# Optimization experiments

Measured on AMD Instinct MI355X. Metric: run time of the kernel, lower is better.

## Reference

```python
import jax, jax.numpy as jnp
import numpy as np

B, S, D = 4, 2048, 1024
CTX_LEN, CTX_DIM = 77, 768
H, DH = 16, 64
INNER = H * DH
MULT = 4
EPS = 1e-5


def setup_inputs() -> dict:
    key = jax.random.key(0)
    ks = jax.random.split(key, 14)
    nrm = lambda k, shape: jax.random.normal(k, shape, dtype=jnp.float32) * 0.02
    return {
        "x": jax.random.normal(ks[0], (B, S, D), dtype=jnp.float32),
        "context": jax.random.normal(ks[1], (B, CTX_LEN, CTX_DIM), dtype=jnp.float32),
        "ln1_g": jnp.ones((D,), jnp.float32), "ln1_b": jnp.zeros((D,), jnp.float32),
        "ln2_g": jnp.ones((D,), jnp.float32), "ln2_b": jnp.zeros((D,), jnp.float32),
        "ln3_g": jnp.ones((D,), jnp.float32), "ln3_b": jnp.zeros((D,), jnp.float32),
        "a1_wq": nrm(ks[2], (D, INNER)), "a1_wk": nrm(ks[3], (D, INNER)),
        "a1_wv": nrm(ks[4], (D, INNER)), "a1_wo": nrm(ks[5], (INNER, D)),
        "a1_bo": jnp.zeros((D,), jnp.float32),
        "a2_wq": nrm(ks[6], (D, INNER)), "a2_wk": nrm(ks[7], (CTX_DIM, INNER)),
        "a2_wv": nrm(ks[8], (CTX_DIM, INNER)), "a2_wo": nrm(ks[9], (INNER, D)),
        "a2_bo": jnp.zeros((D,), jnp.float32),
        "ff_w1": nrm(ks[10], (D, D * MULT * 2)), "ff_b1": jnp.zeros((D * MULT * 2,), jnp.float32),
        "ff_w2": nrm(ks[11], (D * MULT, D)), "ff_b2": jnp.zeros((D,), jnp.float32),
    }


def _layernorm(x, g, b):
    mu = jnp.mean(x, axis=-1, keepdims=True)
    var = jnp.var(x, axis=-1, keepdims=True)
    return (x - mu) * jax.lax.rsqrt(var + EPS) * g + b


def _attn(xq, xkv, wq, wk, wv, wo, bo):
    b, sq, _ = xq.shape
    sk = xkv.shape[1]
    q = (xq @ wq).reshape(b, sq, H, DH)
    k = (xkv @ wk).reshape(b, sk, H, DH)
    v = (xkv @ wv).reshape(b, sk, H, DH)
    score = jnp.einsum('bqhd,bkhd->bhqk', q, k) * (DH ** -0.5)
    w = jax.nn.softmax(score, axis=-1)
    o = jnp.einsum('bhqk,bkhd->bqhd', w, v).reshape(b, sq, INNER)
    return o @ wo + bo


def _block(x, context, ln1_g, ln1_b, ln2_g, ln2_b, ln3_g, ln3_b,
           a1_wq, a1_wk, a1_wv, a1_wo, a1_bo,
           a2_wq, a2_wk, a2_wv, a2_wo, a2_bo,
           ff_w1, ff_b1, ff_w2, ff_b2):
    # self-attention
    x = _attn(_layernorm(x, ln1_g, ln1_b), _layernorm(x, ln1_g, ln1_b),
              a1_wq, a1_wk, a1_wv, a1_wo, a1_bo) + x
    # cross-attention
    x = _attn(_layernorm(x, ln2_g, ln2_b), context,
              a2_wq, a2_wk, a2_wv, a2_wo, a2_bo) + x
    # GeGLU feed-forward
    h = _layernorm(x, ln3_g, ln3_b) @ ff_w1 + ff_b1
    u, gate = jnp.split(h, 2, axis=-1)
    x = (u * jax.nn.gelu(gate, approximate=False)) @ ff_w2 + ff_b2 + x
    return x


def reference(x, context, ln1_g, ln1_b, ln2_g, ln2_b, ln3_g, ln3_b,
              a1_wq, a1_wk, a1_wv, a1_wo, a1_bo,
              a2_wq, a2_wk, a2_wv, a2_wo, a2_bo,
              ff_w1, ff_b1, ff_w2, ff_b2):
    return _block(x, context, ln1_g, ln1_b, ln2_g, ln2_b, ln3_g, ln3_b,
                  a1_wq, a1_wk, a1_wv, a1_wo, a1_bo,
                  a2_wq, a2_wk, a2_wv, a2_wo, a2_bo,
                  ff_w1, ff_b1, ff_w2, ff_b2)
```

## Files before the change

### kernel.cpp

```cpp
#include <hip/hip_runtime.h>
#include <hip/hip_bf16.h>
#include <math.h>

typedef __bf16 bf16;
typedef __bf16 bf16x8 __attribute__((ext_vector_type(8)));
typedef float f32x4 __attribute__((ext_vector_type(4)));

#define MFMA(a, b, c) __builtin_amdgcn_mfma_f32_16x16x32_bf16((a), (b), (c), 0, 0, 0)

static __device__ __forceinline__ void gl16(const bf16* g, bf16* l) {
  __builtin_amdgcn_global_load_lds(
      (const __attribute__((address_space(1))) void*)g,
      (__attribute__((address_space(3))) void*)l, 16, 0, 0);
}

static __device__ __forceinline__ bf16x8 bzero8() {
  bf16x8 v;
#pragma unroll
  for (int i = 0; i < 8; ++i) v[i] = (bf16)0.0f;
  return v;
}

__global__ void k_transpose_cvt(const float* __restrict__ W, bf16* __restrict__ Wt,
                                int K, int N) {
  __shared__ float tile[32][33];
  int k0 = blockIdx.x * 32, n0 = blockIdx.y * 32;
  int tx = threadIdx.x & 31, ty = threadIdx.x >> 5;
  for (int i = ty; i < 32; i += 8)
    tile[i][tx] = W[(size_t)(k0 + i) * N + (n0 + tx)];
  __syncthreads();
  for (int i = ty; i < 32; i += 8)
    Wt[(size_t)(n0 + i) * K + (k0 + tx)] = (bf16)tile[tx][i];
}

__global__ void k_cvt(const float* __restrict__ in, bf16* __restrict__ out, int n) {
  int i = blockIdx.x * 256 + threadIdx.x;
  if (i < n) out[i] = (bf16)in[i];
}

__global__ void k_layernorm(const float* __restrict__ x, const float* __restrict__ g,
                            const float* __restrict__ b, bf16* __restrict__ out) {
  int row = blockIdx.x;
  float4 v = ((const float4*)(x + (size_t)row * 1024))[threadIdx.x];
  float s = v.x + v.y + v.z + v.w;
  float ss = v.x * v.x + v.y * v.y + v.z * v.z + v.w * v.w;
#pragma unroll
  for (int off = 1; off < 64; off <<= 1) {
    s += __shfl_xor(s, off);
    ss += __shfl_xor(ss, off);
  }
  __shared__ float sm[4], sm2[4];
  int w = threadIdx.x >> 6;
  if ((threadIdx.x & 63) == 0) { sm[w] = s; sm2[w] = ss; }
  __syncthreads();
  s = sm[0] + sm[1] + sm[2] + sm[3];
  ss = sm2[0] + sm2[1] + sm2[2] + sm2[3];
  float mu = s * (1.0f / 1024.0f);
  float var = ss * (1.0f / 1024.0f) - mu * mu;
  float rs = rsqrtf(var + 1e-5f);
  float4 gg = ((const float4*)g)[threadIdx.x];
  float4 bb = ((const float4*)b)[threadIdx.x];
  bf16* o = out + (size_t)row * 1024 + threadIdx.x * 4;
  o[0] = (bf16)((v.x - mu) * rs * gg.x + bb.x);
  o[1] = (bf16)((v.y - mu) * rs * gg.y + bb.y);
  o[2] = (bf16)((v.z - mu) * rs * gg.z + bb.z);
  o[3] = (bf16)((v.w - mu) * rs * gg.w + bb.w);
}

template <int EPI>
__global__ __launch_bounds__(256, 2)
void k_gemm_bt(const bf16* __restrict__ A, const bf16* __restrict__ Bt,
               const float* __restrict__ bias, const float* __restrict__ res,
               void* __restrict__ Cp, int M, int N, int K) {
  __shared__ __attribute__((aligned(16))) bf16 As[128 * 32];
  __shared__ __attribute__((aligned(16))) bf16 Bs[128 * 32];
  int m0 = blockIdx.x * 128, n0 = blockIdx.y * 128;
  int tid = threadIdx.x, lane = tid & 63, wave = tid >> 6;
  int wm = (wave >> 1) * 64, wn = (wave & 1) * 64;
  int quad = lane >> 4, l15 = lane & 15;
  f32x4 acc[4][4];
#pragma unroll
  for (int i = 0; i < 4; ++i)
#pragma unroll
    for (int j = 0; j < 4; ++j)
#pragma unroll
      for (int r = 0; r < 4; ++r) acc[i][j][r] = 0.0f;
  int srow = wave * 16 + (lane >> 2), scol = (lane & 3) * 8;
  const bf16* ga = A + (size_t)(m0 + srow) * K + scol;
  const bf16* gb = Bt + (size_t)(n0 + srow) * K + scol;
  bf16* la = As + srow * 32 + scol;
  bf16* lb = Bs + srow * 32 + scol;
  for (int k0 = 0; k0 < K; k0 += 32) {
    gl16(ga, la);
    gl16(ga + (size_t)64 * K, la + 64 * 32);
    gl16(gb, lb);
    gl16(gb + (size_t)64 * K, lb + 64 * 32);
    ga += 32; gb += 32;
    __syncthreads();
    bf16x8 af[4], bfr[4];
#pragma unroll
    for (int i = 0; i < 4; ++i) af[i] = *(const bf16x8*)(&As[(wm + i * 16 + l15) * 32 + quad * 8]);
#pragma unroll
    for (int i = 0; i < 4; ++i) bfr[i] = *(const bf16x8*)(&Bs[(wn + i * 16 + l15) * 32 + quad * 8]);
#pragma unroll
    for (int mi = 0; mi < 4; ++mi)
#pragma unroll
      for (int ni = 0; ni < 4; ++ni)
        acc[mi][ni] = MFMA(af[mi], bfr[ni], acc[mi][ni]);
    __syncthreads();
  }
#pragma unroll
  for (int mi = 0; mi < 4; ++mi) {
#pragma unroll
    for (int r = 0; r < 4; ++r) {
      int row = m0 + wm + mi * 16 + quad * 4 + r;
      if (row >= M) continue;
#pragma unroll
      for (int ni = 0; ni < 4; ++ni) {
        int col = n0 + wn + ni * 16 + l15;
        float v = acc[mi][ni][r];
        if (EPI == 0) {
          ((bf16*)Cp)[(size_t)row * N + col] = (bf16)v;
        } else {
          ((float*)Cp)[(size_t)row * N + col] =
              v + bias[col] + res[(size_t)row * N + col];
        }
      }
    }
  }
}

__global__ __launch_bounds__(256, 2)
void k_gemm_geglu(const bf16* __restrict__ A, const bf16* __restrict__ W1t,
                  const float* __restrict__ b1, bf16* __restrict__ Hg,
                  int M, int K) {
  __shared__ __attribute__((aligned(16))) bf16 As[128 * 32];
  __shared__ __attribute__((aligned(16))) bf16 Bu[64 * 32];
  __shared__ __attribute__((aligned(16))) bf16 Bg[64 * 32];
  const int N = 4096;
  int m0 = blockIdx.x * 128, n0 = blockIdx.y * 64;
  int tid = threadIdx.x, lane = tid & 63, wave = tid >> 6;
  int wm = (wave >> 1) * 64, wn = (wave & 1) * 32;
  int quad = lane >> 4, l15 = lane & 15;
  f32x4 accu[4][2], accg[4][2];
#pragma unroll
  for (int i = 0; i < 4; ++i)
#pragma unroll
    for (int j = 0; j < 2; ++j)
#pragma unroll
      for (int r = 0; r < 4; ++r) { accu[i][j][r] = 0.0f; accg[i][j][r] = 0.0f; }
  int srow = wave * 16 + (lane >> 2), scol = (lane & 3) * 8;
  const bf16* ga = A + (size_t)(m0 + srow) * K + scol;
  const bf16* gu = W1t + (size_t)(n0 + srow) * K + scol;
  const bf16* gg = W1t + (size_t)(n0 + srow + 4096) * K + scol;
  bf16* la = As + srow * 32 + scol;
  bf16* lu = Bu + srow * 32 + scol;
  bf16* lg = Bg + srow * 32 + scol;
  for (int k0 = 0; k0 < K; k0 += 32) {
    gl16(ga, la);
    gl16(ga + (size_t)64 * K, la + 64 * 32);
    gl16(gu, lu);
    gl16(gg, lg);
    ga += 32; gu += 32; gg += 32;
    __syncthreads();
    bf16x8 af[4], bu[2], bg[2];
#pragma unroll
    for (int i = 0; i < 4; ++i) af[i] = *(const bf16x8*)(&As[(wm + i * 16 + l15) * 32 + quad * 8]);
#pragma unroll
    for (int i = 0; i < 2; ++i) bu[i] = *(const bf16x8*)(&Bu[(wn + i * 16 + l15) * 32 + quad * 8]);
#pragma unroll
    for (int i = 0; i < 2; ++i) bg[i] = *(const bf16x8*)(&Bg[(wn + i * 16 + l15) * 32 + quad * 8]);
#pragma unroll
    for (int mi = 0; mi < 4; ++mi)
#pragma unroll
      for (int ni = 0; ni < 2; ++ni) {
        accu[mi][ni] = MFMA(af[mi], bu[ni], accu[mi][ni]);
        accg[mi][ni] = MFMA(af[mi], bg[ni], accg[mi][ni]);
      }
    __syncthreads();
  }
#pragma unroll
  for (int mi = 0; mi < 4; ++mi)
#pragma unroll
    for (int r = 0; r < 4; ++r) {
      int row = m0 + wm + mi * 16 + quad * 4 + r;
#pragma unroll
      for (int ni = 0; ni < 2; ++ni) {
        int col = n0 + wn + ni * 16 + l15;
        float u = accu[mi][ni][r] + b1[col];
        float g = accg[mi][ni][r] + b1[col + 4096];
        float ge = 0.5f * g * (1.0f + erff(g * 0.70710678118654752f));
        Hg[(size_t)row * N + col] = (bf16)(u * ge);
      }
    }
}

__global__ __launch_bounds__(256, 2)
void k_flash(const bf16* __restrict__ Q, const bf16* __restrict__ Kb,
             const bf16* __restrict__ Vb, bf16* __restrict__ O,
             int Sq, int Sk, int kvrows) {
  __shared__ __attribute__((aligned(16))) bf16 Qs[64][72];
  __shared__ __attribute__((aligned(16))) bf16 Ks[64][72];
  __shared__ __attribute__((aligned(16))) bf16 Vt[64][72];
  __shared__ __attribute__((aligned(16))) bf16 Ps[4][16][72];
  int qt = blockIdx.x, h = blockIdx.y, b = blockIdx.z;
  int tid = threadIdx.x, lane = tid & 63, wave = tid >> 6;
  int quad = lane >> 4, l15 = lane & 15;
  {
    int r = tid >> 2, c0 = (tid & 3) * 16;
    const bf16* src = Q + (size_t)(b * Sq + qt * 64 + r) * 1024 + h * 64 + c0;
    *(bf16x8*)(&Qs[r][c0]) = *(const bf16x8*)(src);
    *(bf16x8*)(&Qs[r][c0 + 8]) = *(const bf16x8*)(src + 8);
  }
  float m_r[4], l_r[4];
  f32x4 acc_o[4];
#pragma unroll
  for (int r = 0; r < 4; ++r) { m_r[r] = -1e30f; l_r[r] = 0.0f; }
#pragma unroll
  for (int ni = 0; ni < 4; ++ni)
#pragma unroll
    for (int r = 0; r < 4; ++r) acc_o[ni][r] = 0.0f;

  for (int k0 = 0; k0 < Sk; k0 += 64) {
    {
      int r = tid >> 2, c0 = (tid & 3) * 16;
      int krow = k0 + r;
      bf16x8 k1 = bzero8(), k2 = bzero8(), v1 = bzero8(), v2 = bzero8();
      if (krow < Sk) {
        const bf16* ks = Kb + (size_t)(b * kvrows + krow) * 1024 + h * 64 + c0;
        k1 = *(const bf16x8*)ks;
        k2 = *(const bf16x8*)(ks + 8);
        const bf16* vs = Vb + (size_t)(b * kvrows + krow) * 1024 + h * 64 + c0;
        v1 = *(const bf16x8*)vs;
        v2 = *(const bf16x8*)(vs + 8);
      }
      *(bf16x8*)(&Ks[r][c0]) = k1;
      *(bf16x8*)(&Ks[r][c0 + 8]) = k2;
#pragma unroll
      for (int j = 0; j < 8; ++j) { Vt[c0 + j][r] = v1[j]; Vt[c0 + 8 + j][r] = v2[j]; }
    }
    __syncthreads();

    f32x4 sacc[4];
#pragma unroll
    for (int ni = 0; ni < 4; ++ni)
#pragma unroll
      for (int r = 0; r < 4; ++r) sacc[ni][r] = 0.0f;
#pragma unroll
    for (int ks = 0; ks < 2; ++ks) {
      bf16x8 aq = *(const bf16x8*)(&Qs[wave * 16 + l15][ks * 32 + quad * 8]);
#pragma unroll
      for (int ni = 0; ni < 4; ++ni) {
        bf16x8 bk = *(const bf16x8*)(&Ks[ni * 16 + l15][ks * 32 + quad * 8]);
        sacc[ni] = MFMA(aq, bk, sacc[ni]);
      }
    }
    float s_v[4][4];
#pragma unroll
    for (int ni = 0; ni < 4; ++ni)
#pragma unroll
      for (int r = 0; r < 4; ++r) {
        float sv = sacc[ni][r] * 0.125f;
        if (k0 + ni * 16 + l15 >= Sk) sv = -1e30f;
        s_v[ni][r] = sv;
      }
    float alpha[4];
#pragma unroll
    for (int r = 0; r < 4; ++r) {
      float v = fmaxf(fmaxf(s_v[0][r], s_v[1][r]), fmaxf(s_v[2][r], s_v[3][r]));
#pragma unroll
      for (int off = 1; off < 16; off <<= 1) v = fmaxf(v, __shfl_xor(v, off));
      float mn = fmaxf(m_r[r], v);
      alpha[r] = __expf(m_r[r] - mn);
      m_r[r] = mn;
    }
    float p_v[4][4];
#pragma unroll
    for (int ni = 0; ni < 4; ++ni)
#pragma unroll
      for (int r = 0; r < 4; ++r) p_v[ni][r] = __expf(s_v[ni][r] - m_r[r]);
#pragma unroll
    for (int r = 0; r < 4; ++r) {
      float v = p_v[0][r] + p_v[1][r] + p_v[2][r] + p_v[3][r];
#pragma unroll
      for (int off = 1; off < 16; off <<= 1) v += __shfl_xor(v, off);
      l_r[r] = l_r[r] * alpha[r] + v;
    }
#pragma unroll
    for (int ni = 0; ni < 4; ++ni)
#pragma unroll
      for (int r = 0; r < 4; ++r) acc_o[ni][r] *= alpha[r];
#pragma unroll
    for (int ni = 0; ni < 4; ++ni)
#pragma unroll
      for (int r = 0; r < 4; ++r)
        Ps[wave][quad * 4 + r][ni * 16 + l15] = (bf16)p_v[ni][r];
#pragma unroll
    for (int ks = 0; ks < 2; ++ks) {
      bf16x8 ap = *(const bf16x8*)(&Ps[wave][l15][ks * 32 + quad * 8]);
#pragma unroll
      for (int ni = 0; ni < 4; ++ni) {
        bf16x8 bv = *(const bf16x8*)(&Vt[ni * 16 + l15][ks * 32 + quad * 8]);
        acc_o[ni] = MFMA(ap, bv, acc_o[ni]);
      }
    }
    __syncthreads();
  }
#pragma unroll
  for (int ni = 0; ni < 4; ++ni)
#pragma unroll
    for (int r = 0; r < 4; ++r) {
      int q = qt * 64 + wave * 16 + quad * 4 + r;
      float ov = acc_o[ni][r] / l_r[r];
      O[(size_t)(b * Sq + q) * 1024 + h * 64 + ni * 16 + l15] = (bf16)ov;
    }
}

extern "C" void kernel_launch(void* const* d_in, const int* in_sizes, int n_in,
                              void* d_out, int out_size, void* d_ws, size_t ws_size,
                              hipStream_t stream) {
  (void)in_sizes; (void)n_in; (void)out_size; (void)ws_size;
  const float* x = (const float*)d_in[0];
  const float* ctx = (const float*)d_in[1];
  const float* ln1_g = (const float*)d_in[2];
  const float* ln1_b = (const float*)d_in[3];
  const float* ln2_g = (const float*)d_in[4];
  const float* ln2_b = (const float*)d_in[5];
  const float* ln3_g = (const float*)d_in[6];
  const float* ln3_b = (const float*)d_in[7];
  const float* a1_wq = (const float*)d_in[8];
  const float* a1_wk = (const float*)d_in[9];
  const float* a1_wv = (const float*)d_in[10];
  const float* a1_wo = (const float*)d_in[11];
  const float* a1_bo = (const float*)d_in[12];
  const float* a2_wq = (const float*)d_in[13];
  const float* a2_wk = (const float*)d_in[14];
  const float* a2_wv = (const float*)d_in[15];
  const float* a2_wo = (const float*)d_in[16];
  const float* a2_bo = (const float*)d_in[17];
  const float* ff_w1 = (const float*)d_in[18];
  const float* ff_b1 = (const float*)d_in[19];
  const float* ff_w2 = (const float*)d_in[20];
  const float* ff_b2 = (const float*)d_in[21];
  float* xout = (float*)d_out;

  const int M = 4 * 2048;
  char* ws = (char*)d_ws;
  size_t off = 0;
  auto alloc = [&](size_t elems) -> bf16* {
    bf16* p = (bf16*)(ws + off);
    off += ((elems * sizeof(bf16)) + 255) & ~(size_t)255;
    return p;
  };
  bf16* wq1t = alloc((size_t)1024 * 1024);
  bf16* wk1t = alloc((size_t)1024 * 1024);
  bf16* wv1t = alloc((size_t)1024 * 1024);
  bf16* wo1t = alloc((size_t)1024 * 1024);
  bf16* wq2t = alloc((size_t)1024 * 1024);
  bf16* wk2t = alloc((size_t)1024 * 768);
  bf16* wv2t = alloc((size_t)1024 * 768);
  bf16* wo2t = alloc((size_t)1024 * 1024);
  bf16* w1t = alloc((size_t)8192 * 1024);
  bf16* w2t = alloc((size_t)1024 * 4096);
  bf16* lnb = alloc((size_t)M * 1024);
  bf16* qb = alloc((size_t)M * 1024);
  bf16* kb = alloc((size_t)M * 1024);
  bf16* vb = alloc((size_t)M * 1024);
  bf16* ab = alloc((size_t)M * 1024);
  bf16* ctxb = alloc((size_t)308 * 768);
  bf16* kcb = alloc((size_t)308 * 1024);
  bf16* vcb = alloc((size_t)308 * 1024);
  bf16* hgb = alloc((size_t)M * 4096);

  hipMemcpyAsync(xout, x, (size_t)M * 1024 * sizeof(float),
                 hipMemcpyDeviceToDevice, stream);

  k_transpose_cvt<<<dim3(32, 32), 256, 0, stream>>>(a1_wq, wq1t, 1024, 1024);
  k_transpose_cvt<<<dim3(32, 32), 256, 0, stream>>>(a1_wk, wk1t, 1024, 1024);
  k_transpose_cvt<<<dim3(32, 32), 256, 0, stream>>>(a1_wv, wv1t, 1024, 1024);
  k_transpose_cvt<<<dim3(32, 32), 256, 0, stream>>>(a1_wo, wo1t, 1024, 1024);
  k_transpose_cvt<<<dim3(32, 32), 256, 0, stream>>>(a2_wq, wq2t, 1024, 1024);
  k_transpose_cvt<<<dim3(24, 32), 256, 0, stream>>>(a2_wk, wk2t, 768, 1024);
  k_transpose_cvt<<<dim3(24, 32), 256, 0, stream>>>(a2_wv, wv2t, 768, 1024);
  k_transpose_cvt<<<dim3(32, 32), 256, 0, stream>>>(a2_wo, wo2t, 1024, 1024);
  k_transpose_cvt<<<dim3(32, 256), 256, 0, stream>>>(ff_w1, w1t, 1024, 8192);
  k_transpose_cvt<<<dim3(128, 32), 256, 0, stream>>>(ff_w2, w2t, 4096, 1024);
  k_cvt<<<(308 * 768 + 255) / 256, 256, 0, stream>>>(ctx, ctxb, 308 * 768);

  k_layernorm<<<M, 256, 0, stream>>>(xout, ln1_g, ln1_b, lnb);
  k_gemm_bt<0><<<dim3(64, 8), 256, 0, stream>>>(lnb, wq1t, nullptr, nullptr, qb, M, 1024, 1024);
  k_gemm_bt<0><<<dim3(64, 8), 256, 0, stream>>>(lnb, wk1t, nullptr, nullptr, kb, M, 1024, 1024);
  k_gemm_bt<0><<<dim3(64, 8), 256, 0, stream>>>(lnb, wv1t, nullptr, nullptr, vb, M, 1024, 1024);
  k_flash<<<dim3(32, 16, 4), 256, 0, stream>>>(qb, kb, vb, ab, 2048, 2048, 2048);
  k_gemm_bt<1><<<dim3(64, 8), 256, 0, stream>>>(ab, wo1t, a1_bo, xout, xout, M, 1024, 1024);

  k_layernorm<<<M, 256, 0, stream>>>(xout, ln2_g, ln2_b, lnb);
  k_gemm_bt<0><<<dim3(64, 8), 256, 0, stream>>>(lnb, wq2t, nullptr, nullptr, qb, M, 1024, 1024);
  k_gemm_bt<0><<<dim3(3, 8), 256, 0, stream>>>(ctxb, wk2t, nullptr, nullptr, kcb, 308, 1024, 768);
  k_gemm_bt<0><<<dim3(3, 8), 256, 0, stream>>>(ctxb, wv2t, nullptr, nullptr, vcb, 308, 1024, 768);
  k_flash<<<dim3(32, 16, 4), 256, 0, stream>>>(qb, kcb, vcb, ab, 2048, 77, 77);
  k_gemm_bt<1><<<dim3(64, 8), 256, 0, stream>>>(ab, wo2t, a2_bo, xout, xout, M, 1024, 1024);

  k_layernorm<<<M, 256, 0, stream>>>(xout, ln3_g, ln3_b, lnb);
  k_gemm_geglu<<<dim3(64, 64), 256, 0, stream>>>(lnb, w1t, ff_b1, hgb, M, 1024);
  k_gemm_bt<1><<<dim3(64, 8), 256, 0, stream>>>(hgb, w2t, ff_b2, xout, xout, M, 1024, 4096);
}
```

Measured before the change: 990.1 us.

## Pre-transpose V globally, keep Q in registers, widen GeGLU tile, MFMA row sums

A new kernel transposes V into a per-head [d][token] layout held in the GeGLU scratch buffer. Flash attention can then load V tiles with vector copies instead of scalar transposed LDS stores. Flash also keeps Q fragments in registers, dropping the Q LDS tile, and computes softmax row sums with an MFMA against a ones vector instead of shuffles. The GeGLU GEMM tile grows to 128 columns, which doubles accumulators per wave and may lower occupancy, and the extra transpose launch adds traffic.

```diff
diff --git a/kernel.cpp b/kernel.cpp
--- a/kernel.cpp
+++ b/kernel.cpp
@@ -31,6 +31,31 @@
   __syncthreads();
   for (int i = ty; i < 32; i += 8)
     Wt[(size_t)(n0 + i) * K + (k0 + tx)] = (bf16)tile[tx][i];
+}
+
+__global__ void k_transpose_v(const bf16* __restrict__ V, bf16* __restrict__ Vt,
+                              int rows, int kvpad) {
+  __shared__ __attribute__((aligned(16))) bf16 tile[64][72];
+  int t0 = blockIdx.x * 64, h = blockIdx.y, b = blockIdx.z;
+  int t = threadIdx.x;
+  int tr = t >> 2, c0 = (t & 3) * 16;
+  int token = t0 + tr;
+  bf16x8 a = bzero8(), bv = bzero8();
+  if (token < rows) {
+    const bf16* src = V + ((size_t)(b * rows + token)) * 1024 + h * 64 + c0;
+    a = *(const bf16x8*)src;
+    bv = *(const bf16x8*)(src + 8);
+  }
+  *(bf16x8*)&tile[tr][c0] = a;
+  *(bf16x8*)&tile[tr][c0 + 8] = bv;
+  __syncthreads();
+  int d = t >> 2, tq = (t & 3) * 16;
+  bf16x8 o1, o2;
+#pragma unroll
+  for (int i = 0; i < 8; ++i) { o1[i] = tile[tq + i][d]; o2[i] = tile[tq + 8 + i][d]; }
+  bf16* dst = Vt + ((size_t)((b * 16 + h) * 64 + d)) * kvpad + t0 + tq;
+  *(bf16x8*)dst = o1;
+  *(bf16x8*)(dst + 8) = o2;
 }
 
 __global__ void k_cvt(const float* __restrict__ in, bf16* __restrict__ out, int n) {
@@ -135,18 +160,18 @@
                   const float* __restrict__ b1, bf16* __restrict__ Hg,
                   int M, int K) {
   __shared__ __attribute__((aligned(16))) bf16 As[128 * 32];
-  __shared__ __attribute__((aligned(16))) bf16 Bu[64 * 32];
-  __shared__ __attribute__((aligned(16))) bf16 Bg[64 * 32];
+  __shared__ __attribute__((aligned(16))) bf16 Bu[128 * 32];
+  __shared__ __attribute__((aligned(16))) bf16 Bg[128 * 32];
   const int N = 4096;
-  int m0 = blockIdx.x * 128, n0 = blockIdx.y * 64;
+  int m0 = blockIdx.x * 128, n0 = blockIdx.y * 128;
   int tid = threadIdx.x, lane = tid & 63, wave = tid >> 6;
-  int wm = (wave >> 1) * 64, wn = (wave & 1) * 32;
+  int wm = (wave >> 1) * 64, wn = (wave & 1) * 64;
   int quad = lane >> 4, l15 = lane & 15;
-  f32x4 accu[4][2], accg[4][2];
+  f32x4 accu[4][4], accg[4][4];
 #pragma unroll
   for (int i = 0; i < 4; ++i)
 #pragma unroll
-    for (int j = 0; j < 2; ++j)
+    for (int j = 0; j < 4; ++j)
 #pragma unroll
       for (int r = 0; r < 4; ++r) { accu[i][j][r] = 0.0f; accg[i][j][r] = 0.0f; }
   int srow = wave * 16 + (lane >> 2), scol = (lane & 3) * 8;
@@ -160,20 +185,22 @@
     gl16(ga, la);
     gl16(ga + (size_t)64 * K, la + 64 * 32);
     gl16(gu, lu);
+    gl16(gu + (size_t)64 * K, lu + 64 * 32);
     gl16(gg, lg);
+    gl16(gg + (size_t)64 * K, lg + 64 * 32);
     ga += 32; gu += 32; gg += 32;
     __syncthreads();
-    bf16x8 af[4], bu[2], bg[2];
+    bf16x8 af[4], bu[4], bg[4];
 #pragma unroll
     for (int i = 0; i < 4; ++i) af[i] = *(const bf16x8*)(&As[(wm + i * 16 + l15) * 32 + quad * 8]);
 #pragma unroll
-    for (int i = 0; i < 2; ++i) bu[i] = *(const bf16x8*)(&Bu[(wn + i * 16 + l15) * 32 + quad * 8]);
-#pragma unroll
-    for (int i = 0; i < 2; ++i) bg[i] = *(const bf16x8*)(&Bg[(wn + i * 16 + l15) * 32 + quad * 8]);
+    for (int i = 0; i < 4; ++i) bu[i] = *(const bf16x8*)(&Bu[(wn + i * 16 + l15) * 32 + quad * 8]);
+#pragma unroll
+    for (int i = 0; i < 4; ++i) bg[i] = *(const bf16x8*)(&Bg[(wn + i * 16 + l15) * 32 + quad * 8]);
 #pragma unroll
     for (int mi = 0; mi < 4; ++mi)
 #pragma unroll
-      for (int ni = 0; ni < 2; ++ni) {
+      for (int ni = 0; ni < 4; ++ni) {
         accu[mi][ni] = MFMA(af[mi], bu[ni], accu[mi][ni]);
         accg[mi][ni] = MFMA(af[mi], bg[ni], accg[mi][ni]);
       }
@@ -185,7 +212,7 @@
     for (int r = 0; r < 4; ++r) {
       int row = m0 + wm + mi * 16 + quad * 4 + r;
 #pragma unroll
-      for (int ni = 0; ni < 2; ++ni) {
+      for (int ni = 0; ni < 4; ++ni) {
         int col = n0 + wn + ni * 16 + l15;
         float u = accu[mi][ni][r] + b1[col];
         float g = accg[mi][ni][r] + b1[col + 4096];
@@ -197,21 +224,21 @@
 
 __global__ __launch_bounds__(256, 2)
 void k_flash(const bf16* __restrict__ Q, const bf16* __restrict__ Kb,
-             const bf16* __restrict__ Vb, bf16* __restrict__ O,
-             int Sq, int Sk, int kvrows) {
-  __shared__ __attribute__((aligned(16))) bf16 Qs[64][72];
+             const bf16* __restrict__ VtG, bf16* __restrict__ O,
+             int Sq, int Sk, int kvrows, int kvpad) {
   __shared__ __attribute__((aligned(16))) bf16 Ks[64][72];
-  __shared__ __attribute__((aligned(16))) bf16 Vt[64][72];
+  __shared__ __attribute__((aligned(16))) bf16 Vs[64][72];
   __shared__ __attribute__((aligned(16))) bf16 Ps[4][16][72];
   int qt = blockIdx.x, h = blockIdx.y, b = blockIdx.z;
   int tid = threadIdx.x, lane = tid & 63, wave = tid >> 6;
   int quad = lane >> 4, l15 = lane & 15;
-  {
-    int r = tid >> 2, c0 = (tid & 3) * 16;
-    const bf16* src = Q + (size_t)(b * Sq + qt * 64 + r) * 1024 + h * 64 + c0;
-    *(bf16x8*)(&Qs[r][c0]) = *(const bf16x8*)(src);
-    *(bf16x8*)(&Qs[r][c0 + 8]) = *(const bf16x8*)(src + 8);
-  }
+  const bf16* qsrc = Q + (size_t)(b * Sq + qt * 64 + wave * 16 + l15) * 1024 + h * 64 + quad * 8;
+  bf16x8 aq0 = *(const bf16x8*)qsrc;
+  bf16x8 aq1 = *(const bf16x8*)(qsrc + 32);
+  bf16x8 ones8;
+#pragma unroll
+  for (int i = 0; i < 8; ++i) ones8[i] = (bf16)1.0f;
+
   float m_r[4], l_r[4];
   f32x4 acc_o[4];
 #pragma unroll
@@ -221,23 +248,24 @@
 #pragma unroll
     for (int r = 0; r < 4; ++r) acc_o[ni][r] = 0.0f;
 
+  int tr = tid >> 2, c0 = (tid & 3) * 16;
+  const bf16* vrow = VtG + ((size_t)((b * 16 + h) * 64 + tr)) * kvpad + c0;
+
   for (int k0 = 0; k0 < Sk; k0 += 64) {
     {
-      int r = tid >> 2, c0 = (tid & 3) * 16;
-      int krow = k0 + r;
-      bf16x8 k1 = bzero8(), k2 = bzero8(), v1 = bzero8(), v2 = bzero8();
+      int krow = k0 + tr;
+      bf16x8 k1 = bzero8(), k2 = bzero8();
       if (krow < Sk) {
         const bf16* ks = Kb + (size_t)(b * kvrows + krow) * 1024 + h * 64 + c0;
         k1 = *(const bf16x8*)ks;
         k2 = *(const bf16x8*)(ks + 8);
-        const bf16* vs = Vb + (size_t)(b * kvrows + krow) * 1024 + h * 64 + c0;
-        v1 = *(const bf16x8*)vs;
-        v2 = *(const bf16x8*)(vs + 8);
       }
-      *(bf16x8*)(&Ks[r][c0]) = k1;
-      *(bf16x8*)(&Ks[r][c0 + 8]) = k2;
-#pragma unroll
-      for (int j = 0; j < 8; ++j) { Vt[c0 + j][r] = v1[j]; Vt[c0 + 8 + j][r] = v2[j]; }
+      *(bf16x8*)(&Ks[tr][c0]) = k1;
+      *(bf16x8*)(&Ks[tr][c0 + 8]) = k2;
+      bf16x8 v1 = *(const bf16x8*)(vrow + k0);
+      bf16x8 v2 = *(const bf16x8*)(vrow + k0 + 8);
+      *(bf16x8*)(&Vs[tr][c0]) = v1;
+      *(bf16x8*)(&Vs[tr][c0 + 8]) = v2;
     }
     __syncthreads();
 
@@ -247,13 +275,11 @@
 #pragma unroll
       for (int r = 0; r < 4; ++r) sacc[ni][r] = 0.0f;
 #pragma unroll
-    for (int ks = 0; ks < 2; ++ks) {
-      bf16x8 aq = *(const bf16x8*)(&Qs[wave * 16 + l15][ks * 32 + quad * 8]);
-#pragma unroll
-      for (int ni = 0; ni < 4; ++ni) {
-        bf16x8 bk = *(const bf16x8*)(&Ks[ni * 16 + l15][ks * 32 + quad * 8]);
-        sacc[ni] = MFMA(aq, bk, sacc[ni]);
-      }
+    for (int ni = 0; ni < 4; ++ni) {
+      bf16x8 bk0 = *(const bf16x8*)(&Ks[ni * 16 + l15][quad * 8]);
+      bf16x8 bk1 = *(const bf16x8*)(&Ks[ni * 16 + l15][32 + quad * 8]);
+      sacc[ni] = MFMA(aq0, bk0, sacc[ni]);
+      sacc[ni] = MFMA(aq1, bk1, sacc[ni]);
     }
     float s_v[4][4];
 #pragma unroll
@@ -274,35 +300,28 @@
       alpha[r] = __expf(m_r[r] - mn);
       m_r[r] = mn;
     }
-    float p_v[4][4];
 #pragma unroll
     for (int ni = 0; ni < 4; ++ni)
 #pragma unroll
-      for (int r = 0; r < 4; ++r) p_v[ni][r] = __expf(s_v[ni][r] - m_r[r]);
-#pragma unroll
-    for (int r = 0; r < 4; ++r) {
-      float v = p_v[0][r] + p_v[1][r] + p_v[2][r] + p_v[3][r];
-#pragma unroll
-      for (int off = 1; off < 16; off <<= 1) v += __shfl_xor(v, off);
-      l_r[r] = l_r[r] * alpha[r] + v;
-    }
-#pragma unroll
-    for (int ni = 0; ni < 4; ++ni)
+      for (int r = 0; r < 4; ++r)
+        Ps[wave][quad * 4 + r][ni * 16 + l15] = (bf16)__expf(s_v[ni][r] - m_r[r]);
+    bf16x8 ap0 = *(const bf16x8*)(&Ps[wave][l15][quad * 8]);
+    bf16x8 ap1 = *(const bf16x8*)(&Ps[wave][l15][32 + quad * 8]);
+    f32x4 psum;
+#pragma unroll
+    for (int r = 0; r < 4; ++r) psum[r] = 0.0f;
+    psum = MFMA(ap0, ones8, psum);
+    psum = MFMA(ap1, ones8, psum);
+#pragma unroll
+    for (int r = 0; r < 4; ++r) l_r[r] = l_r[r] * alpha[r] + psum[r];
+#pragma unroll
+    for (int ni = 0; ni < 4; ++ni) {
 #pragma unroll
       for (int r = 0; r < 4; ++r) acc_o[ni][r] *= alpha[r];
-#pragma unroll
-    for (int ni = 0; ni < 4; ++ni)
-#pragma unroll
-      for (int r = 0; r < 4; ++r)
-        Ps[wave][quad * 4 + r][ni * 16 + l15] = (bf16)p_v[ni][r];
-#pragma unroll
-    for (int ks = 0; ks < 2; ++ks) {
-      bf16x8 ap = *(const bf16x8*)(&Ps[wave][l15][ks * 32 + quad * 8]);
-#pragma unroll
-      for (int ni = 0; ni < 4; ++ni) {
-        bf16x8 bv = *(const bf16x8*)(&Vt[ni * 16 + l15][ks * 32 + quad * 8]);
-        acc_o[ni] = MFMA(ap, bv, acc_o[ni]);
-      }
+      bf16x8 bv0 = *(const bf16x8*)(&Vs[ni * 16 + l15][quad * 8]);
+      bf16x8 bv1 = *(const bf16x8*)(&Vs[ni * 16 + l15][32 + quad * 8]);
+      acc_o[ni] = MFMA(ap0, bv0, acc_o[ni]);
+      acc_o[ni] = MFMA(ap1, bv1, acc_o[ni]);
     }
     __syncthreads();
   }
@@ -371,6 +390,8 @@
   bf16* kcb = alloc((size_t)308 * 1024);
   bf16* vcb = alloc((size_t)308 * 1024);
   bf16* hgb = alloc((size_t)M * 4096);
+  bf16* vtb = hgb;
+  bf16* vtcb = hgb + (size_t)4 * 16 * 64 * 2048;
 
   hipMemcpyAsync(xout, x, (size_t)M * 1024 * sizeof(float),
                  hipMemcpyDeviceToDevice, stream);
@@ -391,17 +412,19 @@
   k_gemm_bt<0><<<dim3(64, 8), 256, 0, stream>>>(lnb, wq1t, nullptr, nullptr, qb, M, 1024, 1024);
   k_gemm_bt<0><<<dim3(64, 8), 256, 0, stream>>>(lnb, wk1t, nullptr, nullptr, kb, M, 1024, 1024);
   k_gemm_bt<0><<<dim3(64, 8), 256, 0, stream>>>(lnb, wv1t, nullptr, nullptr, vb, M, 1024, 1024);
-  k_flash<<<dim3(32, 16, 4), 256, 0, stream>>>(qb, kb, vb, ab, 2048, 2048, 2048);
+  k_transpose_v<<<dim3(32, 16, 4), 256, 0, stream>>>(vb, vtb, 2048, 2048);
+  k_flash<<<dim3(32, 16, 4), 256, 0, stream>>>(qb, kb, vtb, ab, 2048, 2048, 2048, 2048);
   k_gemm_bt<1><<<dim3(64, 8), 256, 0, stream>>>(ab, wo1t, a1_bo, xout, xout, M, 1024, 1024);
 
   k_layernorm<<<M, 256, 0, stream>>>(xout, ln2_g, ln2_b, lnb);
   k_gemm_bt<0><<<dim3(64, 8), 256, 0, stream>>>(lnb, wq2t, nullptr, nullptr, qb, M, 1024, 1024);
   k_gemm_bt<0><<<dim3(3, 8), 256, 0, stream>>>(ctxb, wk2t, nullptr, nullptr, kcb, 308, 1024, 768);
   k_gemm_bt<0><<<dim3(3, 8), 256, 0, stream>>>(ctxb, wv2t, nullptr, nullptr, vcb, 308, 1024, 768);
-  k_flash<<<dim3(32, 16, 4), 256, 0, stream>>>(qb, kcb, vcb, ab, 2048, 77, 77);
+  k_transpose_v<<<dim3(2, 16, 4), 256, 0, stream>>>(vcb, vtcb, 77, 128);
+  k_flash<<<dim3(32, 16, 4), 256, 0, stream>>>(qb, kcb, vtcb, ab, 2048, 77, 77, 128);
   k_gemm_bt<1><<<dim3(64, 8), 256, 0, stream>>>(ab, wo2t, a2_bo, xout, xout, M, 1024, 1024);
 
   k_layernorm<<<M, 256, 0, stream>>>(xout, ln3_g, ln3_b, lnb);
-  k_gemm_geglu<<<dim3(64, 64), 256, 0, stream>>>(lnb, w1t, ff_b1, hgb, M, 1024);
+  k_gemm_geglu<<<dim3(64, 32), 256, 0, stream>>>(lnb, w1t, ff_b1, hgb, M, 1024);
   k_gemm_bt<1><<<dim3(64, 8), 256, 0, stream>>>(hgb, w2t, ff_b2, xout, xout, M, 1024, 4096);
 }
```

New measurement: 923.8 us. 1.07x faster.
